# Kernel tuning notes

Measured on AMD Instinct MI355X. Metric: run time of the kernel, lower is better.

Reference implementation:

```python
import jax, jax.numpy as jnp
import numpy as np

N = 50000      # nodes
E = 800000     # edges (before self loops)
DIN = 128      # input_dim
H = 128        # hidden_dim
DOUT = 64      # output_dim
G = 64         # graphs in batch
EATTR = 16     # edge_attr dim (unused by math, kept for signature fidelity)


def _conv_params(key, din, h, scale=0.05):
    ks = jax.random.split(key, 6)
    return dict(
        lin_w=jax.random.normal(ks[0], (din, h), dtype=jnp.float32) * scale,
        lin_b=jnp.zeros((h,), jnp.float32),
        w1=jax.random.normal(ks[1], (2 * h, h), dtype=jnp.float32) * scale,
        b1=jnp.zeros((h,), jnp.float32),
        w2=jax.random.normal(ks[2], (h, h), dtype=jnp.float32) * scale,
        b2=jnp.zeros((h,), jnp.float32),
    )


def setup_inputs() -> dict:
    key = jax.random.key(0)
    ks = jax.random.split(key, 10)
    inp = {
        'x': jax.random.normal(ks[0], (N, DIN), dtype=jnp.float32),
        'edge_index': jax.random.randint(ks[1], (2, E), 0, N),
        'edge_attr': jax.random.normal(ks[2], (E, EATTR), dtype=jnp.float32),
        'batch': jnp.sort(jax.random.randint(ks[3], (N,), 0, G)),
    }
    p1 = _conv_params(ks[4], DIN, H)
    p2 = _conv_params(ks[5], H, H)
    p3 = _conv_params(ks[6], H, H)
    for i, p in enumerate((p1, p2, p3), start=1):
        for k, v in p.items():
            inp[f'c{i}_{k}'] = v
    inp['out_w'] = jax.random.normal(ks[7], (H, DOUT), dtype=jnp.float32) * 0.05
    inp['out_b'] = jnp.zeros((DOUT,), jnp.float32)
    return inp


def mpnn_conv(x, src, dst, lin_w, lin_b, w1, b1, w2, b2):
    # x: [N, din] -> h: [N, H]
    n = x.shape[0]
    h = x @ lin_w + lin_b
    loop = jnp.arange(n)
    s = jnp.concatenate([src, loop])   # x_j (source) indices, self loops appended
    d = jnp.concatenate([dst, loop])   # x_i (target) indices
    z = jnp.concatenate([h[d], h[s]], axis=-1)          # [E+N, 2H]  (cat[x_i, x_j])
    m = jax.nn.relu(z @ w1 + b1) @ w2 + b2              # [E+N, H]
    return jax.ops.segment_sum(m, d, num_segments=n)    # aggr='add' at targets


def reference(x, edge_index, edge_attr, batch,
              c1_lin_w, c1_lin_b, c1_w1, c1_b1, c1_w2, c1_b2,
              c2_lin_w, c2_lin_b, c2_w1, c2_b1, c2_w2, c2_b2,
              c3_lin_w, c3_lin_b, c3_w1, c3_b1, c3_w2, c3_b2,
              out_w, out_b):
    src, dst = edge_index[0], edge_index[1]
    h = jax.nn.relu(mpnn_conv(x, src, dst, c1_lin_w, c1_lin_b, c1_w1, c1_b1, c1_w2, c1_b2))
    h = jax.nn.relu(mpnn_conv(h, src, dst, c2_lin_w, c2_lin_b, c2_w1, c2_b1, c2_w2, c2_b2))
    h = jax.nn.relu(mpnn_conv(h, src, dst, c3_lin_w, c3_lin_b, c3_w1, c3_b1, c3_w2, c3_b2))
    # global_mean_pool over graphs
    sums = jax.ops.segment_sum(h, batch, num_segments=G)                       # [G, H]
    cnts = jax.ops.segment_sum(jnp.ones((h.shape[0],), h.dtype), batch, num_segments=G)
    pooled = sums / jnp.maximum(cnts, 1.0)[:, None]
    return pooled @ out_w + out_b
```

## Files before the change

### kernel.cpp

```cpp
#include <hip/hip_runtime.h>
#include <hip/hip_bf16.h>


typedef _Float16 f16_t;
typedef f16_t f16x2 __attribute__((ext_vector_type(2)));
typedef f16_t f16x8 __attribute__((ext_vector_type(8)));
typedef float f32x4 __attribute__((ext_vector_type(4)));
typedef float f32x2v __attribute__((ext_vector_type(2)));
typedef unsigned int u32;
typedef unsigned short u16;
typedef unsigned char u8;

__device__ __forceinline__ float f16lo(u32 v) {
    return (float)__builtin_bit_cast(f16_t, (u16)(v & 0xffff));
}
__device__ __forceinline__ float f16hi(u32 v) {
    return (float)__builtin_bit_cast(f16_t, (u16)(v >> 16));
}
__device__ __forceinline__ u16 f16b(float x) { return __builtin_bit_cast(u16, (f16_t)x); }
__device__ __forceinline__ u32 f16pack(float x, float y) {
    return (u32)f16b(x) | ((u32)f16b(y) << 16);
}

typedef __attribute__((address_space(1))) void gvoid_t;
typedef __attribute__((address_space(3))) void lvoid_t;
__device__ __forceinline__ void glds16(const void* g, void* l) {
    __builtin_amdgcn_global_load_lds((gvoid_t*)g, (lvoid_t*)l, 16, 0, 0);
}

struct PrepArgs {
    const float* x; f16_t* xb; int totalx;
    const int* ei; int E;
    int* hist; int nbk; int NB;
    const int* batch; int* gstart; int N; int G; int nBat;
    const float* lin_w[3]; const float* lin_b[3];
    const float* w1[3]; const float* b1[3]; const float* w2[3];
    f16_t* linw16;
    f16_t* w1T;
    f16_t* W2t;
    float* bias256c;
};

__global__ __launch_bounds__(256) void prep_kernel(PrepArgs A, int nConvB) {
    __shared__ union { int hist[512]; u16 T16[128 * 130]; } shm;
    const int b = blockIdx.x, tid = threadIdx.x;
    const int nTr = 9, nLw = 48, nBias = 3;
    if (b < nTr) {
        int layer = b / 3, which = b % 3;
        const float* src; f16_t* dst;
        if (which == 0)      { src = A.w1[layer];          dst = A.w1T + layer * 32768; }
        else if (which == 1) { src = A.w1[layer] + 16384;  dst = A.w1T + layer * 32768 + 16384; }
        else                 { src = A.w2[layer];          dst = A.W2t + layer * 16384; }
#pragma unroll
        for (int it = 0; it < 16; ++it) {
            int idx = it * 1024 + tid * 4;
            int r = idx >> 7, c = idx & 127;
            float4 v = *(const float4*)(src + idx);
            *(u32*)&shm.T16[r * 130 + c] = f16pack(v.x, v.y);
            *(u32*)&shm.T16[r * 130 + c + 2] = f16pack(v.z, v.w);
        }
        __syncthreads();
#pragma unroll
        for (int it = 0; it < 32; ++it) {
            int o = it * 256 + tid;
            int j = o >> 6, c = (o & 63) * 2;
            u32 w = (u32)shm.T16[c * 130 + j] | ((u32)shm.T16[(c + 1) * 130 + j] << 16);
            ((u32*)dst)[o] = w;
        }
        return;
    }
    if (b < nTr + nLw) {
        int i = (b - nTr) * 1024 + tid * 4;
        int layer = i >> 14, off = i & 16383;
        float4 v = *(const float4*)(A.lin_w[layer] + off);
        *(uint2*)(A.linw16 + i) = make_uint2(f16pack(v.x, v.y), f16pack(v.z, v.w));
        return;
    }
    if (b < nTr + nLw + nBias) {
        int layer = b - nTr - nLw;
        int j = tid;
        const float* w1p = A.w1[layer];
        const float* wcol = (j < 128) ? (w1p + j) : (w1p + 16384 + (j - 128));
        const float* lbp = A.lin_b[layer];
        float s = (j < 128) ? A.b1[layer][j] : 0.f;
        for (int c = 0; c < 128; ++c) s += lbp[c] * wcol[c * 128];
        A.bias256c[layer * 256 + j] = s;
        return;
    }
    if (b < nTr + nLw + nBias + A.NB) {
        const int bb = b - nTr - nLw - nBias;
        const int nbk = A.nbk, E = A.E;
        for (int i = tid; i < nbk; i += 256) shm.hist[i] = 0;
        __syncthreads();
        const int chunk = (E + A.NB - 1) / A.NB;
        const int e0 = bb * chunk, e1 = min(E, e0 + chunk);
        for (int e = e0 + tid; e < e1; e += 256) atomicAdd(&shm.hist[A.ei[E + e] >> 7], 1);
        __syncthreads();
        for (int i = tid; i < nbk; i += 256) A.hist[(size_t)bb * nbk + i] = shm.hist[i];
        return;
    }
    if (b < nTr + nLw + nBias + A.NB + A.nBat) {
        int n = (b - nTr - nLw - nBias - A.NB) * 256 + tid;
        if (n >= A.N) return;
        int b1 = A.batch[n];
        if (n == 0) {
            for (int g = 0; g <= b1; ++g) A.gstart[g] = 0;
        } else {
            int b0 = A.batch[n - 1];
            if (b0 != b1)
                for (int g = b0 + 1; g <= b1; ++g) A.gstart[g] = n;
        }
        if (n == A.N - 1)
            for (int g = b1 + 1; g <= A.G; ++g) A.gstart[g] = A.N;
        return;
    }
    int i = ((b - nTr - nLw - nBias - A.NB - A.nBat) * 256 + tid) * 4;
    if (i >= A.totalx) return;
    float4 v = *(const float4*)(A.x + i);
    *(uint2*)(A.xb + i) = make_uint2(f16pack(v.x, v.y), f16pack(v.z, v.w));
}

__global__ __launch_bounds__(256) void hscan_kernel(int* __restrict__ hist,
                                                    int* __restrict__ bcnt, int nbk, int NB) {
    __shared__ int sh[256];
    const int b = blockIdx.x, t = threadIdx.x;
    int run = 0;
    for (int c0 = 0; c0 < NB; c0 += 256) {
        int idx = c0 + t;
        int v = (idx < NB) ? hist[(size_t)idx * nbk + b] : 0;
        sh[t] = v;
        __syncthreads();
#pragma unroll
        for (int o = 1; o < 256; o <<= 1) {
            int u = (t >= o) ? sh[t - o] : 0;
            __syncthreads();
            sh[t] += u;
            __syncthreads();
        }
        if (idx < NB) hist[(size_t)idx * nbk + b] = run + sh[t] - v;
        int tot = sh[255];
        __syncthreads();
        run += tot;
    }
    if (t == 0) bcnt[b] = run;
}

__global__ __launch_bounds__(256) void scat_kernel(const int* __restrict__ ei,
                                                   const int* __restrict__ hist,
                                                   u32* __restrict__ bbuf, int E, int NB,
                                                   int nbk, int cap) {
    __shared__ int basep[512];
    __shared__ int cnt2[512];
    const int bb = blockIdx.x, t = threadIdx.x;
    for (int i = t; i < nbk; i += 256) {
        basep[i] = hist[(size_t)bb * nbk + i];
        cnt2[i] = 0;
    }
    __syncthreads();
    const int chunk = (E + NB - 1) / NB;
    const int e0 = bb * chunk, e1 = min(E, e0 + chunk);
    for (int e = e0 + t; e < e1; e += 256) {
        int dst = ei[E + e], src = ei[e];
        int bkt = dst >> 7;
        int r = atomicAdd(&cnt2[bkt], 1);
        int pp = basep[bkt] + r;
        if (pp < cap) bbuf[(size_t)bkt * cap + pp] = ((u32)(dst & 127) << 16) | (u32)src;
    }
}

__global__ __launch_bounds__(128) void part2_kernel(const u32* __restrict__ bbuf,
                                                    const int* __restrict__ bcnt,
                                                    int* __restrict__ row_ptr,
                                                    float* __restrict__ cntp1f,
                                                    int* __restrict__ bsumB, int cap, int N) {
    __shared__ int ldeg[128];
    __shared__ int sh[128];
    const int b = blockIdx.x, t = threadIdx.x;
    ldeg[t] = 0;
    __syncthreads();
    const int cnt = min(bcnt[b], cap);
    const u32* p = bbuf + (size_t)b * cap;
    for (int i = t; i < cnt; i += 128) atomicAdd(&ldeg[p[i] >> 16], 1);
    __syncthreads();
    int d = ldeg[t];
    sh[t] = d;
    __syncthreads();
#pragma unroll
    for (int o = 1; o < 128; o <<= 1) {
        int u = (t >= o) ? sh[t - o] : 0;
        __syncthreads();
        sh[t] += u;
        __syncthreads();
    }
    int node = (b << 7) + t;
    if (node < N) {
        row_ptr[node] = sh[t] - d;
        cntp1f[node] = (float)(d + 1);
    }
    if (t == 127) bsumB[b] = sh[127];
}

__global__ __launch_bounds__(512) void scanb_kernel(const int* __restrict__ bsumB,
                                                    int* __restrict__ bbase,
                                                    int* __restrict__ row_ptr, int nbk, int N) {
    __shared__ int sh[512];
    const int t = threadIdx.x;
    int v = (t < nbk) ? bsumB[t] : 0;
    sh[t] = v;
    __syncthreads();
#pragma unroll
    for (int o = 1; o < 512; o <<= 1) {
        int u = (t >= o) ? sh[t - o] : 0;
        __syncthreads();
        sh[t] += u;
        __syncthreads();
    }
    if (t < nbk) bbase[t] = sh[t] - v;
    if (t == 511) row_ptr[N] = sh[511];
}

__global__ __launch_bounds__(128) void part3_kernel(const u32* __restrict__ bbuf,
                                                    const int* __restrict__ bcnt,
                                                    const int* __restrict__ bbase,
                                                    int* __restrict__ row_ptr,
                                                    u16* __restrict__ colarr, int cap, int N) {
    __shared__ int lcur[128];
    const int b = blockIdx.x, t = threadIdx.x;
    const int node = (b << 7) + t;
    const int bb = bbase[b];
    int rp = 0;
    if (node < N) {
        rp = row_ptr[node] + bb;
        row_ptr[node] = rp;
    }
    lcur[t] = rp;
    __syncthreads();
    const int cnt = min(bcnt[b], cap);
    const u32* p = bbuf + (size_t)b * cap;
    for (int i = t; i < cnt; i += 128) {
        u32 en = p[i];
        int addr = atomicAdd(&lcur[en >> 16], 1);
        colarr[addr] = (u16)(en & 0xffffu);
    }
}

__device__ __forceinline__ void gemm_tile(const f16_t* __restrict__ X,
                                          const f16_t* __restrict__ Wt,
                                          f16_t* __restrict__ Y, int N,
                                          int ldc, int row0) {
    __shared__ f16_t sX[128 * 128];
    __shared__ f16_t sW[128 * 128];
    const int tid = threadIdx.x;
    const int wave = tid >> 6, lane = tid & 63;
#pragma unroll
    for (int it = 0; it < 8; ++it) {
        int idx = it * 256 + tid;
        int r = idx >> 4, c8 = idx & 15;
        int gr = row0 + r;
        if (gr >= N) gr = 0;
        glds16(X + (size_t)gr * 128 + ((c8 ^ (r & 7)) * 8),
               sX + (size_t)(it * 256 + (wave << 6)) * 8);
    }
#pragma unroll
    for (int it = 0; it < 8; ++it) {
        int idx = it * 256 + tid;
        int r = idx >> 4, c8 = idx & 15;
        glds16(Wt + (size_t)r * 128 + ((c8 ^ (r & 7)) * 8),
               sW + (size_t)(it * 256 + (wave << 6)) * 8);
    }
    __syncthreads();
    const int m = lane & 15, q = lane >> 4;
    const int sw = m & 7;
    f32x4 acc[2][8];
#pragma unroll
    for (int rt = 0; rt < 2; ++rt)
#pragma unroll
        for (int t = 0; t < 8; ++t) acc[rt][t] = (f32x4){0.f, 0.f, 0.f, 0.f};
#pragma unroll
    for (int kk = 0; kk < 4; ++kk) {
        const int g = (kk * 4 + q) ^ sw;
        f16x8 a0 = *(const f16x8*)(&sX[(wave * 32 + m) * 128 + g * 8]);
        f16x8 a1 = *(const f16x8*)(&sX[(wave * 32 + 16 + m) * 128 + g * 8]);
#pragma unroll
        for (int t = 0; t < 8; ++t) {
            f16x8 bfr = *(const f16x8*)(&sW[(t * 16 + m) * 128 + g * 8]);
            acc[0][t] = __builtin_amdgcn_mfma_f32_16x16x32_f16(a0, bfr, acc[0][t], 0, 0, 0);
            acc[1][t] = __builtin_amdgcn_mfma_f32_16x16x32_f16(a1, bfr, acc[1][t], 0, 0, 0);
        }
    }
#pragma unroll
    for (int t = 0; t < 8; ++t) {
        int col = t * 16 + m;
#pragma unroll
        for (int rt = 0; rt < 2; ++rt) {
#pragma unroll
            for (int j = 0; j < 4; ++j) {
                int r = row0 + wave * 32 + rt * 16 + q * 4 + j;
                if (r < N) Y[(size_t)r * ldc + col] = (f16_t)acc[rt][t][j];
            }
        }
    }
}

__global__ __launch_bounds__(256) void compose_kernel(const f16_t* __restrict__ w1T,
                                                      const f16_t* __restrict__ linw16,
                                                      f16_t* __restrict__ W12ct) {
    int layer = blockIdx.x >> 1, rb = blockIdx.x & 1;
    gemm_tile(w1T + layer * 32768, linw16 + layer * 16384, W12ct + layer * 32768, 256, 128,
              rb * 128);
}

template <int NT>
__global__ __launch_bounds__(512, 1) void gemm_persist(
    const f16_t* __restrict__ X, const f16_t* __restrict__ Wt,
    const float* __restrict__ bias, const float* __restrict__ bias2,
    const float* __restrict__ rowscale, f16_t* __restrict__ Y, u8* __restrict__ Y8,
    int N, int relu_flag, int ntiles) {
    __shared__ f16_t sW[NT * 16 * 128];
    __shared__ f16_t sX[2][128 * 128];
    const int tid = threadIdx.x;
    const int wave = tid >> 6, lane = tid & 63;
    const int m = lane & 15, q = lane >> 4, sw = m & 7;
    constexpr int NR = (NT == 16) ? 2 : 1;
    const int rb0 = (NT == 16) ? ((wave & 3) * 32) : (wave * 16);
    const int chalf = (NT == 16) ? (wave >> 2) : 0;

#pragma unroll
    for (int it = 0; it < NT / 2; ++it) {
        int idx = it * 512 + tid;
        int r = idx >> 4, c8 = idx & 15;
        glds16(Wt + (size_t)r * 128 + ((c8 ^ (r & 7)) * 8),
               sW + (size_t)(it * 512 + (wave << 6)) * 8);
    }
    float bvv[8], b2vv[8];
#pragma unroll
    for (int t2 = 0; t2 < 8; ++t2) {
        int colb = chalf * 128 + t2 * 16 + m;
        bvv[t2] = bias ? bias[colb] : 0.f;
        b2vv[t2] = bias2 ? bias2[colb] : 0.f;
    }
    int t = blockIdx.x;
    {
        int row0 = t * 128;
#pragma unroll
        for (int it = 0; it < 4; ++it) {
            int idx = it * 512 + tid;
            int r = idx >> 4, c8 = idx & 15;
            int gr = row0 + r;
            if (gr >= N) gr = 0;
            glds16(X + (size_t)gr * 128 + ((c8 ^ (r & 7)) * 8),
                   sX[0] + (size_t)(it * 512 + (wave << 6)) * 8);
        }
    }
    __syncthreads();
    int cur = 0;
    for (; t < ntiles; t += gridDim.x) {
        const int row0 = t * 128;
        const int tn = t + gridDim.x;
        f16_t* sXc = sX[cur];
        if (tn < ntiles) {
            const int r0n = tn * 128;
            f16_t* sXn = sX[cur ^ 1];
#pragma unroll
            for (int it = 0; it < 4; ++it) {
                int idx = it * 512 + tid;
                int r = idx >> 4, c8 = idx & 15;
                int gr = r0n + r;
                if (gr >= N) gr = 0;
                glds16(X + (size_t)gr * 128 + ((c8 ^ (r & 7)) * 8),
                       sXn + (size_t)(it * 512 + (wave << 6)) * 8);
            }
        }
        f32x4 acc[NR][8];
#pragma unroll
        for (int rt = 0; rt < NR; ++rt)
#pragma unroll
            for (int t2 = 0; t2 < 8; ++t2) acc[rt][t2] = (f32x4){0.f, 0.f, 0.f, 0.f};
#pragma unroll
        for (int kk = 0; kk < 4; ++kk) {
            const int g = (kk * 4 + q) ^ sw;
            f16x8 a0 = *(const f16x8*)(&sXc[(rb0 + m) * 128 + g * 8]);
            f16x8 a1{};
            if constexpr (NR == 2) a1 = *(const f16x8*)(&sXc[(rb0 + 16 + m) * 128 + g * 8]);
#pragma unroll
            for (int t2 = 0; t2 < 8; ++t2) {
                f16x8 bfr =
                    *(const f16x8*)(&sW[(size_t)(chalf * 128 + t2 * 16 + m) * 128 + g * 8]);
                acc[0][t2] = __builtin_amdgcn_mfma_f32_16x16x32_f16(a0, bfr, acc[0][t2], 0, 0, 0);
                if constexpr (NR == 2)
                    acc[1][t2] =
                        __builtin_amdgcn_mfma_f32_16x16x32_f16(a1, bfr, acc[1][t2], 0, 0, 0);
            }
        }
        if (NT == 16) __syncthreads();
        f16_t* region = sXc + wave * 16 * 128;
#pragma unroll
        for (int rt = 0; rt < NR; ++rt) {
            float rs[4];
#pragma unroll
            for (int j = 0; j < 4; ++j) {
                int gr = row0 + rb0 + rt * 16 + q * 4 + j;
                rs[j] = (bias2 && gr < N) ? rowscale[gr] : 0.f;
            }
#pragma unroll
            for (int t2 = 0; t2 < 8; ++t2) {
#pragma unroll
                for (int j = 0; j < 4; ++j) {
                    int rl2 = q * 4 + j;
                    float v = acc[rt][t2][j] + bvv[t2];
                    if (bias2) v += rs[j] * b2vv[t2];
                    if (relu_flag) v = fmaxf(v, 0.f);
                    region[rl2 * 128 + ((t2 * 16 + m) ^ ((rl2 & 4) << 3))] = (f16_t)v;
                }
            }
#pragma unroll
            for (int it2 = 0; it2 < 4; ++it2) {
                int i = it2 * 64 + lane;
                int rl = i >> 4, c8 = i & 15;
                int gr = row0 + rb0 + rt * 16 + rl;
                const f16_t* rp = &region[rl * 128 + ((c8 ^ (rl & 4)) * 8)];
                if (NT == 16 && chalf == 1) {
                    const u32* p = (const u32*)rp;
                    u32 lo = __builtin_amdgcn_cvt_pk_fp8_f32(f16lo(p[0]), f16hi(p[0]), 0u, false);
                    lo = __builtin_amdgcn_cvt_pk_fp8_f32(f16lo(p[1]), f16hi(p[1]), lo, true);
                    u32 hi = __builtin_amdgcn_cvt_pk_fp8_f32(f16lo(p[2]), f16hi(p[2]), 0u, false);
                    hi = __builtin_amdgcn_cvt_pk_fp8_f32(f16lo(p[3]), f16hi(p[3]), hi, true);
                    if (gr < N) *(uint2*)(Y8 + (size_t)gr * 128 + c8 * 8) = make_uint2(lo, hi);
                } else {
                    uint4 v4 = *(const uint4*)rp;
                    if (gr < N) *(uint4*)(Y + (size_t)gr * 128 + c8 * 8) = v4;
                }
            }
        }
        __syncthreads();
        cur ^= 1;
    }
}

__global__ __launch_bounds__(256) void gather_kernel(const f16_t* __restrict__ aArr,
                                                     const u8* __restrict__ b8,
                                                     const int* __restrict__ row_ptr,
                                                     const u16* __restrict__ colarr,
                                                     f16_t* __restrict__ q, int N) {
    int wid = (blockIdx.x * 256 + threadIdx.x) >> 6;
    int lane = threadIdx.x & 63;
    if (wid >= N) return;
    const int g = lane >> 4, l = lane & 15;
    uint4 A = ((const uint4*)aArr)[(size_t)wid * 16 + l];
    float a0 = f16lo(A.x), a1 = f16hi(A.x), a2 = f16lo(A.y), a3 = f16hi(A.y);
    float a4 = f16lo(A.z), a5 = f16hi(A.z), a6 = f16lo(A.w), a7 = f16hi(A.w);
    float c0 = 0.f, c1 = 0.f, c2 = 0.f, c3 = 0.f, c4 = 0.f, c5 = 0.f, c6 = 0.f, c7 = 0.f;
    const uint2* b8u = (const uint2*)b8;
    auto accum = [&](uint2 B) {
        f32x2v p0 = __builtin_amdgcn_cvt_pk_f32_fp8(B.x, false);
        f32x2v p1 = __builtin_amdgcn_cvt_pk_f32_fp8(B.x, true);
        f32x2v p2 = __builtin_amdgcn_cvt_pk_f32_fp8(B.y, false);
        f32x2v p3 = __builtin_amdgcn_cvt_pk_f32_fp8(B.y, true);
        c0 += fmaxf(a0 + p0.x, 0.f); c1 += fmaxf(a1 + p0.y, 0.f);
        c2 += fmaxf(a2 + p1.x, 0.f); c3 += fmaxf(a3 + p1.y, 0.f);
        c4 += fmaxf(a4 + p2.x, 0.f); c5 += fmaxf(a5 + p2.y, 0.f);
        c6 += fmaxf(a6 + p3.x, 0.f); c7 += fmaxf(a7 + p3.y, 0.f);
    };
    if (g == 0) accum(b8u[(size_t)wid * 16 + l]);
    const int e0 = row_ptr[wid], e1 = row_ptr[wid + 1];
    for (int e = e0; e < e1; e += 16) {
#pragma unroll
        for (int s = 0; s < 4; ++s) {
            int idx = e + s * 4 + g;
            int src = colarr[min(idx, e1 - 1)];
            uint2 B = b8u[(size_t)src * 16 + l];
            if (idx < e1) accum(B);
        }
    }
#pragma unroll
    for (int off = 16; off < 64; off <<= 1) {
        c0 += __shfl_xor(c0, off); c1 += __shfl_xor(c1, off);
        c2 += __shfl_xor(c2, off); c3 += __shfl_xor(c3, off);
        c4 += __shfl_xor(c4, off); c5 += __shfl_xor(c5, off);
        c6 += __shfl_xor(c6, off); c7 += __shfl_xor(c7, off);
    }
    if (g == 0) {
        uint4 o;
        o.x = f16pack(c0, c1); o.y = f16pack(c2, c3);
        o.z = f16pack(c4, c5); o.w = f16pack(c6, c7);
        ((uint4*)q)[(size_t)wid * 16 + l] = o;
    }
}

__global__ __launch_bounds__(256) void pool_kernel(const f16_t* __restrict__ agg,
                                                   const int* __restrict__ gstart,
                                                   float* __restrict__ pooled) {
    __shared__ float red[4][128];
    const int g = blockIdx.x >> 3, part = blockIdx.x & 7;
    const int tid = threadIdx.x, wave = tid >> 6, lane = tid & 63;
    const int lo = gstart[g], hi = gstart[g + 1];
    const int cnt = hi - lo;
    const int len = (cnt + 7) >> 3;
    const int n0 = lo + part * len, n1 = min(hi, n0 + len);
    const u32* au = (const u32*)agg;
    float sx = 0.f, sy = 0.f;
#pragma unroll 4
    for (int n = n0 + wave; n < n1; n += 4) {
        u32 v = au[(size_t)n * 64 + lane];
        sx += f16lo(v);
        sy += f16hi(v);
    }
    red[wave][lane * 2] = sx;
    red[wave][lane * 2 + 1] = sy;
    __syncthreads();
    if (wave == 0) {
        float a = red[0][lane * 2] + red[1][lane * 2] + red[2][lane * 2] + red[3][lane * 2];
        float b = red[0][lane * 2 + 1] + red[1][lane * 2 + 1] + red[2][lane * 2 + 1] +
                  red[3][lane * 2 + 1];
        atomicAdd(&pooled[g * 128 + lane * 2], a);
        atomicAdd(&pooled[g * 128 + lane * 2 + 1], b);
    }
}

__global__ __launch_bounds__(256) void final_kernel(const float* __restrict__ pooled,
                                                    const int* __restrict__ gstart,
                                                    const float* __restrict__ out_w,
                                                    const float* __restrict__ out_b,
                                                    float* __restrict__ out) {
    __shared__ float red[256];
    const int g = blockIdx.x, tid = threadIdx.x;
    const int o = tid & 63, part = tid >> 6;
    float s = 0.f;
#pragma unroll
    for (int kk = 0; kk < 32; ++kk) {
        int k = part * 32 + kk;
        s += pooled[g * 128 + k] * out_w[k * 64 + o];
    }
    red[tid] = s;
    __syncthreads();
    if (part == 0) {
        float c = fmaxf((float)(gstart[g + 1] - gstart[g]), 1.0f);
        float tot = red[o] + red[o + 64] + red[o + 128] + red[o + 192];
        out[g * 64 + o] = tot / c + out_b[o];
    }
}

extern "C" void kernel_launch(void* const* d_in, const int* in_sizes, int n_in, void* d_out,
                              int out_size, void* d_ws, size_t ws_size, hipStream_t stream) {
    const float* x = (const float*)d_in[0];
    const int* ei = (const int*)d_in[1];
    const int* batch = (const int*)d_in[3];
    const float* cw[3][6];
    for (int l = 0; l < 3; ++l)
        for (int j = 0; j < 6; ++j) cw[l][j] = (const float*)d_in[4 + l * 6 + j];
    const float* out_w = (const float*)d_in[22];
    const float* out_b = (const float*)d_in[23];
    float* out = (float*)d_out;

    const int N = in_sizes[0] / 128;
    const int E = in_sizes[1] / 2;
    const int G = out_size / 64;
    const int nbk = (N + 127) >> 7;
    const int NB = 416;
    const int cap = E / nbk + 512;
    const int nBat = (N + 255) / 256;

    char* base = (char*)d_ws;
    size_t off = 0;
    auto alloc = [&](size_t b) { size_t o = off; off += (b + 255) & ~(size_t)255; return o; };
    float* pooled = (float*)(base + alloc((size_t)G * 128 * 4));
    const size_t zero_bytes = off;
    int* gstart = (int*)(base + alloc((size_t)(G + 1) * 4));
    int* hist = (int*)(base + alloc((size_t)NB * nbk * 4));
    int* bcnt = (int*)(base + alloc((size_t)nbk * 4));
    int* bsumB = (int*)(base + alloc((size_t)nbk * 4));
    int* bbase = (int*)(base + alloc((size_t)nbk * 4));
    int* row_ptr = (int*)(base + alloc((size_t)(N + 1) * 4));
    float* cntp1f = (float*)(base + alloc((size_t)N * 4));
    u16* colarr = (u16*)(base + alloc((size_t)E * 2));
    u32* bbuf = (u32*)(base + alloc((size_t)nbk * cap * 4));
    f16_t* xb = (f16_t*)(base + alloc((size_t)N * 128 * 2));
    f16_t* q = (f16_t*)(base + alloc((size_t)N * 128 * 2));
    f16_t* aArr = (f16_t*)(base + alloc((size_t)N * 128 * 2));
    u8* b8 = (u8*)(base + alloc((size_t)N * 128));
    f16_t* linw16 = (f16_t*)(base + alloc(3 * 16384 * 2));
    f16_t* w1T = (f16_t*)(base + alloc(3 * 32768 * 2));
    f16_t* W12ct = (f16_t*)(base + alloc(3 * 32768 * 2));
    f16_t* W2t = (f16_t*)(base + alloc(3 * 16384 * 2));
    float* bias256c = (float*)(base + alloc(3 * 256 * 4));
    (void)ws_size; (void)n_in;

    hipMemsetAsync(d_ws, 0, zero_bytes, stream);

    PrepArgs pa;
    pa.x = x; pa.xb = xb; pa.totalx = N * 128;
    pa.ei = ei; pa.E = E;
    pa.hist = hist; pa.nbk = nbk; pa.NB = NB;
    pa.batch = batch; pa.gstart = gstart; pa.N = N; pa.G = G; pa.nBat = nBat;
    for (int l = 0; l < 3; ++l) {
        pa.lin_w[l] = cw[l][0]; pa.lin_b[l] = cw[l][1];
        pa.w1[l] = cw[l][2]; pa.b1[l] = cw[l][3]; pa.w2[l] = cw[l][4];
    }
    pa.linw16 = linw16; pa.w1T = w1T; pa.W2t = W2t; pa.bias256c = bias256c;
    const int nConvB = (N * 128 / 4 + 255) / 256;
    prep_kernel<<<9 + 48 + 3 + NB + nBat + nConvB, 256, 0, stream>>>(pa, nConvB);

    compose_kernel<<<6, 256, 0, stream>>>(w1T, linw16, W12ct);

    hscan_kernel<<<nbk, 256, 0, stream>>>(hist, bcnt, nbk, NB);
    scat_kernel<<<NB, 256, 0, stream>>>(ei, hist, bbuf, E, NB, nbk, cap);
    part2_kernel<<<nbk, 128, 0, stream>>>(bbuf, bcnt, row_ptr, cntp1f, bsumB, cap, N);
    scanb_kernel<<<1, 512, 0, stream>>>(bsumB, bbase, row_ptr, nbk, N);
    part3_kernel<<<nbk, 128, 0, stream>>>(bbuf, bcnt, bbase, row_ptr, colarr, cap, N);

    const int ntiles = (N + 127) >> 7;
    const int pgrid = (ntiles < 256) ? ntiles : 256;
    const f16_t* Xin = xb;
    for (int l = 0; l < 3; ++l) {
        gemm_persist<16><<<pgrid, 512, 0, stream>>>(Xin, W12ct + l * 32768,
                                                    bias256c + l * 256, nullptr, nullptr,
                                                    aArr, b8, N, 0, ntiles);
        gather_kernel<<<(N * 64 + 255) / 256, 256, 0, stream>>>(aArr, b8, row_ptr, colarr, q, N);
        gemm_persist<8><<<pgrid, 512, 0, stream>>>(q, W2t + l * 16384, nullptr, cw[l][5],
                                                   cntp1f, xb, nullptr, N, 1, ntiles);
        Xin = xb;
    }

    pool_kernel<<<G * 8, 256, 0, stream>>>(Xin, gstart, pooled);
    final_kernel<<<G, 256, 0, stream>>>(pooled, gstart, out_w, out_b, out);
}
```

Measured before the change: 379.6 us.

## Fuse per-layer output GEMM with next layer's input GEMM in one persistent kernel

Adds a persistent kernel that computes a layer's second MLP GEMM with bias, degree scaling and ReLU, keeps the result in shared memory, then immediately runs the next layer's composed first GEMM on it. This avoids writing the intermediate node features to global memory and reading them back, and removes one launch per layer boundary. It uses about 128 KB of shared memory per block for both weight matrices plus the activation tile, which limits occupancy to one block per CU.

```diff
diff --git a/kernel.cpp b/kernel.cpp
--- a/kernel.cpp
+++ b/kernel.cpp
@@ -434,6 +434,138 @@
         }
         __syncthreads();
         cur ^= 1;
+    }
+}
+
+__global__ __launch_bounds__(512, 1) void fused_g8_g16(
+    const f16_t* __restrict__ q, const f16_t* __restrict__ W2t,
+    const float* __restrict__ b2, const float* __restrict__ cntp1f,
+    const f16_t* __restrict__ W12ct, const float* __restrict__ bias16,
+    f16_t* __restrict__ aArr, u8* __restrict__ Y8, int N, int ntiles) {
+    __shared__ f16_t sW2[128 * 128];
+    __shared__ f16_t sW12[256 * 128];
+    __shared__ f16_t sX[128 * 128];
+    const int tid = threadIdx.x;
+    const int wave = tid >> 6, lane = tid & 63;
+    const int m = lane & 15, qd = lane >> 4, sw = m & 7;
+    const int chalf = wave >> 2, rb0c = (wave & 3) * 32;
+
+#pragma unroll
+    for (int it = 0; it < 4; ++it) {
+        int idx = it * 512 + tid;
+        int r = idx >> 4, c8 = idx & 15;
+        glds16(W2t + (size_t)r * 128 + ((c8 ^ (r & 7)) * 8),
+               sW2 + (size_t)(it * 512 + (wave << 6)) * 8);
+    }
+#pragma unroll
+    for (int it = 0; it < 8; ++it) {
+        int idx = it * 512 + tid;
+        int r = idx >> 4, c8 = idx & 15;
+        glds16(W12ct + (size_t)r * 128 + ((c8 ^ (r & 7)) * 8),
+               sW12 + (size_t)(it * 512 + (wave << 6)) * 8);
+    }
+    float b2v[8], bv16[8];
+#pragma unroll
+    for (int t2 = 0; t2 < 8; ++t2) {
+        b2v[t2] = b2[t2 * 16 + m];
+        bv16[t2] = bias16[chalf * 128 + t2 * 16 + m];
+    }
+
+    for (int t = blockIdx.x; t < ntiles; t += gridDim.x) {
+        const int row0 = t * 128;
+#pragma unroll
+        for (int it = 0; it < 4; ++it) {
+            int idx = it * 512 + tid;
+            int r = idx >> 4, c8 = idx & 15;
+            int gr = row0 + r;
+            if (gr >= N) gr = 0;
+            glds16(q + (size_t)gr * 128 + ((c8 ^ (r & 7)) * 8),
+                   sX + (size_t)(it * 512 + (wave << 6)) * 8);
+        }
+        __syncthreads();
+
+        f32x4 accB[8];
+#pragma unroll
+        for (int t2 = 0; t2 < 8; ++t2) accB[t2] = (f32x4){0.f, 0.f, 0.f, 0.f};
+#pragma unroll
+        for (int kk = 0; kk < 4; ++kk) {
+            const int g = (kk * 4 + qd) ^ sw;
+            f16x8 a0 = *(const f16x8*)(&sX[(wave * 16 + m) * 128 + g * 8]);
+#pragma unroll
+            for (int t2 = 0; t2 < 8; ++t2) {
+                f16x8 bfr = *(const f16x8*)(&sW2[(t2 * 16 + m) * 128 + g * 8]);
+                accB[t2] = __builtin_amdgcn_mfma_f32_16x16x32_f16(a0, bfr, accB[t2], 0, 0, 0);
+            }
+        }
+        float rs[4];
+#pragma unroll
+        for (int j = 0; j < 4; ++j) {
+            int gr = row0 + wave * 16 + qd * 4 + j;
+            rs[j] = (gr < N) ? cntp1f[gr] : 0.f;
+        }
+#pragma unroll
+        for (int t2 = 0; t2 < 8; ++t2) {
+#pragma unroll
+            for (int j = 0; j < 4; ++j) {
+                int rr = wave * 16 + qd * 4 + j;
+                float v = fmaxf(accB[t2][j] + rs[j] * b2v[t2], 0.f);
+                sX[rr * 128 + (((2 * t2 + (m >> 3)) ^ (rr & 7)) * 8 + (m & 7))] = (f16_t)v;
+            }
+        }
+        __syncthreads();
+
+        f32x4 accC[2][8];
+#pragma unroll
+        for (int rt = 0; rt < 2; ++rt)
+#pragma unroll
+            for (int t2 = 0; t2 < 8; ++t2) accC[rt][t2] = (f32x4){0.f, 0.f, 0.f, 0.f};
+#pragma unroll
+        for (int kk = 0; kk < 4; ++kk) {
+            const int g = (kk * 4 + qd) ^ sw;
+            f16x8 a0 = *(const f16x8*)(&sX[(rb0c + m) * 128 + g * 8]);
+            f16x8 a1 = *(const f16x8*)(&sX[(rb0c + 16 + m) * 128 + g * 8]);
+#pragma unroll
+            for (int t2 = 0; t2 < 8; ++t2) {
+                f16x8 bfr =
+                    *(const f16x8*)(&sW12[(size_t)(chalf * 128 + t2 * 16 + m) * 128 + g * 8]);
+                accC[0][t2] = __builtin_amdgcn_mfma_f32_16x16x32_f16(a0, bfr, accC[0][t2], 0, 0, 0);
+                accC[1][t2] = __builtin_amdgcn_mfma_f32_16x16x32_f16(a1, bfr, accC[1][t2], 0, 0, 0);
+            }
+        }
+        __syncthreads();
+
+        f16_t* region = sX + wave * 16 * 128;
+#pragma unroll
+        for (int rt = 0; rt < 2; ++rt) {
+#pragma unroll
+            for (int t2 = 0; t2 < 8; ++t2) {
+#pragma unroll
+                for (int j = 0; j < 4; ++j) {
+                    int rl2 = qd * 4 + j;
+                    float v = accC[rt][t2][j] + bv16[t2];
+                    region[rl2 * 128 + ((t2 * 16 + m) ^ ((rl2 & 4) << 3))] = (f16_t)v;
+                }
+            }
+#pragma unroll
+            for (int it2 = 0; it2 < 4; ++it2) {
+                int i = it2 * 64 + lane;
+                int rl = i >> 4, c8 = i & 15;
+                int gr = row0 + rb0c + rt * 16 + rl;
+                const f16_t* rp = &region[rl * 128 + ((c8 ^ (rl & 4)) * 8)];
+                if (chalf == 1) {
+                    const u32* p = (const u32*)rp;
+                    u32 lo = __builtin_amdgcn_cvt_pk_fp8_f32(f16lo(p[0]), f16hi(p[0]), 0u, false);
+                    lo = __builtin_amdgcn_cvt_pk_fp8_f32(f16lo(p[1]), f16hi(p[1]), lo, true);
+                    u32 hi = __builtin_amdgcn_cvt_pk_fp8_f32(f16lo(p[2]), f16hi(p[2]), 0u, false);
+                    hi = __builtin_amdgcn_cvt_pk_fp8_f32(f16lo(p[3]), f16hi(p[3]), hi, true);
+                    if (gr < N) *(uint2*)(Y8 + (size_t)gr * 128 + c8 * 8) = make_uint2(lo, hi);
+                } else {
+                    uint4 v4 = *(const uint4*)rp;
+                    if (gr < N) *(uint4*)(aArr + (size_t)gr * 128 + c8 * 8) = v4;
+                }
+            }
+        }
+        __syncthreads();
     }
 }
 
@@ -610,17 +742,22 @@
 
     const int ntiles = (N + 127) >> 7;
     const int pgrid = (ntiles < 256) ? ntiles : 256;
-    const f16_t* Xin = xb;
+
+    gemm_persist<16><<<pgrid, 512, 0, stream>>>(xb, W12ct, bias256c, nullptr, nullptr,
+                                                aArr, b8, N, 0, ntiles);
     for (int l = 0; l < 3; ++l) {
-        gemm_persist<16><<<pgrid, 512, 0, stream>>>(Xin, W12ct + l * 32768,
-                                                    bias256c + l * 256, nullptr, nullptr,
-                                                    aArr, b8, N, 0, ntiles);
         gather_kernel<<<(N * 64 + 255) / 256, 256, 0, stream>>>(aArr, b8, row_ptr, colarr, q, N);
-        gemm_persist<8><<<pgrid, 512, 0, stream>>>(q, W2t + l * 16384, nullptr, cw[l][5],
-                                                   cntp1f, xb, nullptr, N, 1, ntiles);
-        Xin = xb;
-    }
-
-    pool_kernel<<<G * 8, 256, 0, stream>>>(Xin, gstart, pooled);
+        if (l < 2) {
+            fused_g8_g16<<<pgrid, 512, 0, stream>>>(q, W2t + l * 16384, cw[l][5], cntp1f,
+                                                    W12ct + (l + 1) * 32768,
+                                                    bias256c + (l + 1) * 256, aArr, b8, N,
+                                                    ntiles);
+        } else {
+            gemm_persist<8><<<pgrid, 512, 0, stream>>>(q, W2t + l * 16384, nullptr, cw[l][5],
+                                                       cntp1f, xb, nullptr, N, 1, ntiles);
+        }
+    }
+
+    pool_kernel<<<G * 8, 256, 0, stream>>>(xb, gstart, pooled);
     final_kernel<<<G, 256, 0, stream>>>(pooled, gstart, out_w, out_b, out);
 }
```

After: 368.8 us, median of 2. 2.8% less time.
